# Performance work log

Hardware: AMD Instinct MI355X
Metric: run time of the kernel (lower is better)

Reference implementation:

```python
import jax, jax.numpy as jnp
import numpy as np

# near_sym_a (5,7)-tap biorthogonal analysis filters used by DTCWT level 1
_H0O = np.array([-0.05, 0.25, 0.5, 0.25, -0.05], dtype=np.float32)
_H1O = np.array([-0.0107143, 0.0535714, 0.2607143, -0.6071429,
                 0.2607143, 0.0535714, -0.0107143], dtype=np.float32)

MAGBIAS = np.float32(0.01)


def _filt(x, h, axis):
    """Depthwise 1D correlation of NCHW x along `axis` (2=H rows, 3=W cols)
    with symmetric (half-sample reflect) padding; output same spatial size
    (odd-length filters)."""
    m = h.shape[0] // 2
    pad = [(0, 0)] * 4
    pad[axis] = (m, m)
    xp = jnp.pad(x, pad, mode='symmetric')
    n, c, hh, ww = xp.shape
    k = h.reshape(1, 1, -1, 1) if axis == 2 else h.reshape(1, 1, 1, -1)
    y = jax.lax.conv_general_dilated(
        xp.reshape(n * c, 1, hh, ww), k, (1, 1), 'VALID',
        dimension_numbers=('NCHW', 'OIHW', 'NCHW'))
    return y.reshape(n, c, y.shape[2], y.shape[3])


def _q2c(y):
    # quads -> two complex subimages: ((a-d) + j(b+c), (a+d) + j(b-c)) / sqrt(2)
    y = y * np.float32(1.0 / np.sqrt(2.0))
    a = y[..., 0::2, 0::2]
    b = y[..., 0::2, 1::2]
    c = y[..., 1::2, 0::2]
    d = y[..., 1::2, 1::2]
    return (a - d, b + c), (a + d, b - c)


def _scat_j1(x, h0o, h1o, magbias):
    # level-1 DTCWT: separable biorthogonal filtering (no decimation)
    lo = _filt(x, h0o, 3)   # row lowpass  (along W)
    hi = _filt(x, h1o, 3)   # row highpass
    ll = _filt(lo, h0o, 2)  # (N,C,H,W) lowpass
    lh = _filt(lo, h1o, 2)
    hl = _filt(hi, h0o, 2)
    hh = _filt(hi, h1o, 2)
    # quads -> 6 oriented complex subbands at half resolution
    (d15r, d15i), (d165r, d165i) = _q2c(lh)
    (d45r, d45i), (d135r, d135i) = _q2c(hh)
    (d75r, d75i), (d105r, d105i) = _q2c(hl)
    reals = jnp.stack([d15r, d45r, d75r, d105r, d135r, d165r], axis=1)  # (N,6,C,H/2,W/2)
    imags = jnp.stack([d15i, d45i, d75i, d105i, d135i, d165i], axis=1)
    # smoothed complex magnitude nonlinearity
    r = jnp.sqrt(reals * reals + imags * imags + magbias * magbias) - magbias
    # 2x2 average pool of lowpass
    n, c, hh_, ww_ = ll.shape
    ll = ll.reshape(n, c, hh_ // 2, 2, ww_ // 2, 2).mean(axis=(3, 5))
    b_, _, c_, h_, w_ = r.shape
    r = r.reshape(b_, 6 * c_, h_, w_)
    return ll, r


def setup_inputs() -> dict:
    key = jax.random.key(0)
    x = jax.random.normal(key, (32, 64, 128, 128), dtype=jnp.float32)
    # non-trainable wavelet filter "parameters" (fixed near_sym_a taps)
    return {"x": x, "h0o": jnp.asarray(_H0O), "h1o": jnp.asarray(_H1O)}


def reference(x, h0o, h1o):
    # H, W are even here so the odd-size edge-replication branch is a no-op
    return _scat_j1(x, h0o, h1o, MAGBIAS)
```

## Files before the change

### kernel.cpp

```cpp
#include <hip/hip_runtime.h>
#include <math.h>

#define W 128
#define LROWS 38
#define TILE_IN 32
#define TILE_OUT 16
#define NTILES 4

typedef float f4 __attribute__((ext_vector_type(4)));
typedef float f2 __attribute__((ext_vector_type(2)));

__device__ __forceinline__ int refl128(int i) {
    i = (i < 0) ? (-1 - i) : i;
    return (i > 127) ? (255 - i) : i;
}

__device__ __forceinline__ f2 mag2(f2 re, f2 im) {
    f2 t = re * re + im * im + 1.0e-4f;
    f2 s = __builtin_elementwise_sqrt(t);
    return s - 0.01f;
}

__device__ __forceinline__ void st2v(float* p, f2 v) {
    __builtin_nontemporal_store(v, (f2*)p);
}

__device__ __forceinline__ void q2c(f4 t, f4 b, f2& mneg, f2& mpos) {
    const f2 e  = __builtin_shufflevector(t, t, 0, 2);
    const f2 eo = __builtin_shufflevector(t, t, 1, 3);
    const f2 o  = __builtin_shufflevector(b, b, 1, 3);
    const f2 oo = __builtin_shufflevector(b, b, 0, 2);
    mneg = mag2(e - o, eo + oo);
    mpos = mag2(e + o, eo - oo);
}

__global__ __launch_bounds__(256) void scat_j1_kernel(
    const float* __restrict__ x,
    float* __restrict__ out_ll,
    float* __restrict__ out_r)
{
    __shared__ float slo[LROWS][W];
    __shared__ float shi[LROWS][W];

    const int raw   = blockIdx.x;
    const int L_id  = (raw & 7) * 1024 + (raw >> 3);
    const int plane = L_id >> 2;
    const int tile  = L_id & 3;
    const int r0    = tile * TILE_IN;
    const int tid   = threadIdx.x;

    const float* __restrict__ xp = x + (size_t)plane * (W * W);

    {
        const int g  = tid & 31;
        const int rb = tid >> 5;
        #pragma unroll
        for (int it = 0; it < 5; ++it) {
            const int lr = it * 8 + rb;
            if (lr < LROWS) {
                const int q = refl128(r0 - 3 + lr);
                const f4* __restrict__ rv = (const f4*)(xp + (size_t)q * W);
                const f4 B = rv[g];
                f4 A = rv[g > 0 ? g - 1 : 0];
                f4 C = rv[g < 31 ? g + 1 : 31];
                const f4 revB = __builtin_shufflevector(B, B, 3, 2, 1, 0);
                if (g == 0)  A = revB;
                if (g == 31) C = revB;
                const f4 m0 = __builtin_shufflevector(A, B, 1, 2, 3, 4);
                const f4 m1 = __builtin_shufflevector(A, B, 2, 3, 4, 5);
                const f4 m2 = __builtin_shufflevector(A, B, 3, 4, 5, 6);
                const f4 m3 = B;
                const f4 m4 = __builtin_shufflevector(B, C, 1, 2, 3, 4);
                const f4 m5 = __builtin_shufflevector(B, C, 2, 3, 4, 5);
                const f4 m6 = __builtin_shufflevector(B, C, 3, 4, 5, 6);
                const f4 s06 = m0 + m6;
                const f4 s15 = m1 + m5;
                const f4 s24 = m2 + m4;
                const f4 lo4 = -0.05f * s15 + 0.25f * s24 + 0.5f * m3;
                const f4 hi4 = -0.0107143f * s06 + 0.0535714f * s15
                             +  0.2607143f * s24 + -0.6071429f * m3;
                ((f4*)&slo[lr][0])[g] = lo4;
                ((f4*)&shi[lr][0])[g] = hi4;
            }
        }
    }
    __syncthreads();

    const int cp = tid & 31;
    const int Ib = tid >> 5;
    const int R0 = 4 * Ib;
    const int n  = plane >> 6;
    const int ch = plane & 63;

    const float S   = 0.70710678118654752f;
    const float a7  = -0.0107143f * S, b7 = 0.0535714f * S,
                c7  =  0.2607143f * S, d7 = -0.6071429f * S;
    const float a5s = -0.05f * S, b5s = 0.25f * S, c5s = 0.5f * S;
    const float p5a = -0.0125f, p5b = 0.0625f, p5c = 0.125f;

    const int I0 = tile * TILE_OUT + 2 * Ib;
    float* llp = out_ll + (size_t)plane * 4096 + (size_t)I0 * 64 + 2 * cp;
    float* rp  = out_r + ((size_t)(n * 384 + ch)) * 4096 + (size_t)I0 * 64 + 2 * cp;

    {
        f4 v[10];
        #pragma unroll
        for (int t = 0; t < 10; ++t) v[t] = ((const f4*)&slo[R0 + t][0])[cp];
        #pragma unroll
        for (int k = 0; k < 2; ++k) {
            const f4* w = v + 2 * k;
            const f4 s15 = w[1] + w[5], s24 = w[2] + w[4];
            const f4 s26 = w[2] + w[6], s35 = w[3] + w[5];
            const f4 t7 = a7 * (w[0] + w[6]) + b7 * s15 + c7 * s24 + d7 * w[3];
            const f4 bo = a7 * (w[1] + w[7]) + b7 * s26 + c7 * s35 + d7 * w[4];
            f2 m15, m165;
            q2c(t7, bo, m15, m165);
            const f4 lt = p5a * s15 + p5b * s24 + p5c * w[3];
            const f4 lb = p5a * s26 + p5b * s35 + p5c * w[4];
            const f4 sl = lt + lb;
            f2 llv;
            llv.x = sl.x + sl.y;
            llv.y = sl.z + sl.w;
            st2v(llp + k * 64, llv);
            st2v(rp + k * 64 + 0u * 262144u, m15);
            st2v(rp + k * 64 + 5u * 262144u, m165);
        }
    }
    {
        f4 v[10];
        #pragma unroll
        for (int t = 0; t < 10; ++t) v[t] = ((const f4*)&shi[R0 + t][0])[cp];
        #pragma unroll
        for (int k = 0; k < 2; ++k) {
            const f4* w = v + 2 * k;
            const f4 s15 = w[1] + w[5], s24 = w[2] + w[4];
            const f4 s26 = w[2] + w[6], s35 = w[3] + w[5];
            const f4 t7 = a7 * (w[0] + w[6]) + b7 * s15 + c7 * s24 + d7 * w[3];
            const f4 bo = a7 * (w[1] + w[7]) + b7 * s26 + c7 * s35 + d7 * w[4];
            f2 m45, m135;
            q2c(t7, bo, m45, m135);
            const f4 ht = a5s * s15 + b5s * s24 + c5s * w[3];
            const f4 hb = a5s * s26 + b5s * s35 + c5s * w[4];
            f2 m75, m105;
            q2c(ht, hb, m75, m105);
            st2v(rp + k * 64 + 1u * 262144u, m45);
            st2v(rp + k * 64 + 2u * 262144u, m75);
            st2v(rp + k * 64 + 3u * 262144u, m105);
            st2v(rp + k * 64 + 4u * 262144u, m135);
        }
    }
}

extern "C" void kernel_launch(void* const* d_in, const int* in_sizes, int n_in,
                              void* d_out, int out_size, void* d_ws, size_t ws_size,
                              hipStream_t stream) {
    const float* x = (const float*)d_in[0];
    float* out = (float*)d_out;
    float* out_ll = out;
    float* out_r  = out + 8388608;

    dim3 grid(2048 * NTILES);
    dim3 block(256);
    hipLaunchKernelGGL(scat_j1_kernel, grid, block, 0, stream, x, out_ll, out_r);
}
```

Measured before the change: 75.66 us.

## Split block into producer/consumer warps with double-buffered row tiles

Each block now processes half a plane as four 16-row tiles. Half the threads compute row lowpass/highpass into a double-buffered shared array while the other half run column filtering, magnitude and stores on the previous tile. This aims to overlap global loads with the compute-and-store phase. In exchange, the halo-row overhead per tile is larger, only half the threads work in each phase, and extra barriers are added.

```diff
diff --git a/kernel.cpp b/kernel.cpp
--- a/kernel.cpp
+++ b/kernel.cpp
@@ -2,10 +2,10 @@
 #include <math.h>
 
 #define W 128
-#define LROWS 38
-#define TILE_IN 32
-#define TILE_OUT 16
-#define NTILES 4
+#define LROWS 22
+#define TILE_IN 16
+#define TILE_OUT 8
+#define TPB 4
 
 typedef float f4 __attribute__((ext_vector_type(4)));
 typedef float f2 __attribute__((ext_vector_type(2)));
@@ -25,7 +25,7 @@
     __builtin_nontemporal_store(v, (f2*)p);
 }
 
-__device__ __forceinline__ void q2c(f4 t, f4 b, f2& mneg, f2& mpos) {
+__device__ __forceinline__ void q2cm(f4 t, f4 b, f2& mneg, f2& mpos) {
     const f2 e  = __builtin_shufflevector(t, t, 0, 2);
     const f2 eo = __builtin_shufflevector(t, t, 1, 3);
     const f2 o  = __builtin_shufflevector(b, b, 1, 3);
@@ -39,24 +39,39 @@
     float* __restrict__ out_ll,
     float* __restrict__ out_r)
 {
-    __shared__ float slo[LROWS][W];
-    __shared__ float shi[LROWS][W];
+    __shared__ float slo[2][LROWS][W];
+    __shared__ float shi[2][LROWS][W];
 
     const int raw   = blockIdx.x;
-    const int L_id  = (raw & 7) * 1024 + (raw >> 3);
-    const int plane = L_id >> 2;
-    const int tile  = L_id & 3;
-    const int r0    = tile * TILE_IN;
+    const int L_id  = (raw & 7) * 512 + (raw >> 3);
+    const int plane = L_id >> 1;
+    const int half  = L_id & 1;
     const int tid   = threadIdx.x;
+    const bool producer = (tid < 128);
 
+    const int n  = plane >> 6;
+    const int ch = plane & 63;
     const float* __restrict__ xp = x + (size_t)plane * (W * W);
 
-    {
-        const int g  = tid & 31;
-        const int rb = tid >> 5;
+    const int g   = tid & 31;
+    const int rb4 = (tid >> 5) & 3;
+
+    const int ct  = tid & 127;
+    const int cp  = ct & 31;
+    const int Ibh = ct >> 5;
+    const int R0  = 4 * Ibh;
+
+    const float S   = 0.70710678118654752f;
+    const float a7  = -0.0107143f * S, b7 = 0.0535714f * S,
+                c7  =  0.2607143f * S, d7 = -0.6071429f * S;
+    const float a5s = -0.05f * S, b5s = 0.25f * S, c5s = 0.5f * S;
+    const float p5a = -0.0125f, p5b = 0.0625f, p5c = 0.125f;
+
+    auto stage = [&](int buf, int t) {
+        const int r0 = (half * TPB + t) * TILE_IN;
         #pragma unroll
-        for (int it = 0; it < 5; ++it) {
-            const int lr = it * 8 + rb;
+        for (int it = 0; it < 6; ++it) {
+            const int lr = it * 4 + rb4;
             if (lr < LROWS) {
                 const int q = refl128(r0 - 3 + lr);
                 const f4* __restrict__ rv = (const f4*)(xp + (size_t)q * W);
@@ -79,75 +94,77 @@
                 const f4 lo4 = -0.05f * s15 + 0.25f * s24 + 0.5f * m3;
                 const f4 hi4 = -0.0107143f * s06 + 0.0535714f * s15
                              +  0.2607143f * s24 + -0.6071429f * m3;
-                ((f4*)&slo[lr][0])[g] = lo4;
-                ((f4*)&shi[lr][0])[g] = hi4;
+                ((f4*)&slo[buf][lr][0])[g] = lo4;
+                ((f4*)&shi[buf][lr][0])[g] = hi4;
             }
         }
-    }
+    };
+
+    auto consume = [&](int buf, int t) {
+        const int tile_abs = half * TPB + t;
+        const int I0 = tile_abs * TILE_OUT + 2 * Ibh;
+        float* llp = out_ll + (size_t)plane * 4096 + (size_t)I0 * 64 + 2 * cp;
+        float* rp  = out_r + ((size_t)(n * 384 + ch)) * 4096 + (size_t)I0 * 64 + 2 * cp;
+
+        {
+            f4 v[10];
+            #pragma unroll
+            for (int u = 0; u < 10; ++u) v[u] = ((const f4*)&slo[buf][R0 + u][0])[cp];
+            #pragma unroll
+            for (int k = 0; k < 2; ++k) {
+                const f4* w = v + 2 * k;
+                const f4 s15 = w[1] + w[5], s24 = w[2] + w[4];
+                const f4 s26 = w[2] + w[6], s35 = w[3] + w[5];
+                const f4 t7 = a7 * (w[0] + w[6]) + b7 * s15 + c7 * s24 + d7 * w[3];
+                const f4 bo = a7 * (w[1] + w[7]) + b7 * s26 + c7 * s35 + d7 * w[4];
+                f2 m15, m165;
+                q2cm(t7, bo, m15, m165);
+                const f4 lt = p5a * s15 + p5b * s24 + p5c * w[3];
+                const f4 lb = p5a * s26 + p5b * s35 + p5c * w[4];
+                const f4 sl = lt + lb;
+                f2 llv;
+                llv.x = sl.x + sl.y;
+                llv.y = sl.z + sl.w;
+                st2v(llp + k * 64, llv);
+                st2v(rp + k * 64 + 0u * 262144u, m15);
+                st2v(rp + k * 64 + 5u * 262144u, m165);
+            }
+        }
+        {
+            f4 v[10];
+            #pragma unroll
+            for (int u = 0; u < 10; ++u) v[u] = ((const f4*)&shi[buf][R0 + u][0])[cp];
+            #pragma unroll
+            for (int k = 0; k < 2; ++k) {
+                const f4* w = v + 2 * k;
+                const f4 s15 = w[1] + w[5], s24 = w[2] + w[4];
+                const f4 s26 = w[2] + w[6], s35 = w[3] + w[5];
+                const f4 t7 = a7 * (w[0] + w[6]) + b7 * s15 + c7 * s24 + d7 * w[3];
+                const f4 bo = a7 * (w[1] + w[7]) + b7 * s26 + c7 * s35 + d7 * w[4];
+                f2 m45, m135;
+                q2cm(t7, bo, m45, m135);
+                const f4 ht = a5s * s15 + b5s * s24 + c5s * w[3];
+                const f4 hb = a5s * s26 + b5s * s35 + c5s * w[4];
+                f2 m75, m105;
+                q2cm(ht, hb, m75, m105);
+                st2v(rp + k * 64 + 1u * 262144u, m45);
+                st2v(rp + k * 64 + 2u * 262144u, m75);
+                st2v(rp + k * 64 + 3u * 262144u, m105);
+                st2v(rp + k * 64 + 4u * 262144u, m135);
+            }
+        }
+    };
+
+    if (producer) stage(0, 0);
     __syncthreads();
-
-    const int cp = tid & 31;
-    const int Ib = tid >> 5;
-    const int R0 = 4 * Ib;
-    const int n  = plane >> 6;
-    const int ch = plane & 63;
-
-    const float S   = 0.70710678118654752f;
-    const float a7  = -0.0107143f * S, b7 = 0.0535714f * S,
-                c7  =  0.2607143f * S, d7 = -0.6071429f * S;
-    const float a5s = -0.05f * S, b5s = 0.25f * S, c5s = 0.5f * S;
-    const float p5a = -0.0125f, p5b = 0.0625f, p5c = 0.125f;
-
-    const int I0 = tile * TILE_OUT + 2 * Ib;
-    float* llp = out_ll + (size_t)plane * 4096 + (size_t)I0 * 64 + 2 * cp;
-    float* rp  = out_r + ((size_t)(n * 384 + ch)) * 4096 + (size_t)I0 * 64 + 2 * cp;
-
-    {
-        f4 v[10];
-        #pragma unroll
-        for (int t = 0; t < 10; ++t) v[t] = ((const f4*)&slo[R0 + t][0])[cp];
-        #pragma unroll
-        for (int k = 0; k < 2; ++k) {
-            const f4* w = v + 2 * k;
-            const f4 s15 = w[1] + w[5], s24 = w[2] + w[4];
-            const f4 s26 = w[2] + w[6], s35 = w[3] + w[5];
-            const f4 t7 = a7 * (w[0] + w[6]) + b7 * s15 + c7 * s24 + d7 * w[3];
-            const f4 bo = a7 * (w[1] + w[7]) + b7 * s26 + c7 * s35 + d7 * w[4];
-            f2 m15, m165;
-            q2c(t7, bo, m15, m165);
-            const f4 lt = p5a * s15 + p5b * s24 + p5c * w[3];
-            const f4 lb = p5a * s26 + p5b * s35 + p5c * w[4];
-            const f4 sl = lt + lb;
-            f2 llv;
-            llv.x = sl.x + sl.y;
-            llv.y = sl.z + sl.w;
-            st2v(llp + k * 64, llv);
-            st2v(rp + k * 64 + 0u * 262144u, m15);
-            st2v(rp + k * 64 + 5u * 262144u, m165);
+    #pragma unroll
+    for (int t = 0; t < TPB; ++t) {
+        if (producer) {
+            if (t + 1 < TPB) stage((t + 1) & 1, t + 1);
+        } else {
+            consume(t & 1, t);
         }
-    }
-    {
-        f4 v[10];
-        #pragma unroll
-        for (int t = 0; t < 10; ++t) v[t] = ((const f4*)&shi[R0 + t][0])[cp];
-        #pragma unroll
-        for (int k = 0; k < 2; ++k) {
-            const f4* w = v + 2 * k;
-            const f4 s15 = w[1] + w[5], s24 = w[2] + w[4];
-            const f4 s26 = w[2] + w[6], s35 = w[3] + w[5];
-            const f4 t7 = a7 * (w[0] + w[6]) + b7 * s15 + c7 * s24 + d7 * w[3];
-            const f4 bo = a7 * (w[1] + w[7]) + b7 * s26 + c7 * s35 + d7 * w[4];
-            f2 m45, m135;
-            q2c(t7, bo, m45, m135);
-            const f4 ht = a5s * s15 + b5s * s24 + c5s * w[3];
-            const f4 hb = a5s * s26 + b5s * s35 + c5s * w[4];
-            f2 m75, m105;
-            q2c(ht, hb, m75, m105);
-            st2v(rp + k * 64 + 1u * 262144u, m45);
-            st2v(rp + k * 64 + 2u * 262144u, m75);
-            st2v(rp + k * 64 + 3u * 262144u, m105);
-            st2v(rp + k * 64 + 4u * 262144u, m135);
-        }
+        __syncthreads();
     }
 }
 
@@ -159,7 +176,7 @@
     float* out_ll = out;
     float* out_r  = out + 8388608;
 
-    dim3 grid(2048 * NTILES);
+    dim3 grid(2048 * 2);
     dim3 block(256);
     hipLaunchKernelGGL(scat_j1_kernel, grid, block, 0, stream, x, out_ll, out_r);
 }
```

Result: slower. 89.33 us (+18.1%).
